# Kernel optimization log

Hardware: AMD Instinct MI355X
Metric: run time of the kernel (lower is better)

## Reference

```python
import jax, jax.numpy as jnp
import numpy as np

B, L, D_MODEL = 2, 2048, 512
EXPAND = 2
ED = EXPAND * D_MODEL          # d_inner = 1024
N = 16                          # d_state
D_CONV = 4
DT_RANK = (D_MODEL + N - 1) // N  # 32
D_FF = 1024
EPS = 1e-5


def _mamba_params(key, pre):
    ks = jax.random.split(key, 6)
    s = 0.02
    p = {}
    p[pre + 'in_w'] = jax.random.normal(ks[0], (D_MODEL, 2 * ED), jnp.float32) * s
    p[pre + 'conv_w'] = jax.random.normal(ks[1], (ED, 1, D_CONV), jnp.float32) * s
    p[pre + 'conv_b'] = jnp.zeros((ED,), jnp.float32)
    p[pre + 'xproj_w'] = jax.random.normal(ks[2], (ED, DT_RANK + 2 * N), jnp.float32) * s
    p[pre + 'dt_w'] = jax.random.normal(ks[3], (DT_RANK, ED), jnp.float32) * s
    p[pre + 'dt_b'] = jax.random.normal(ks[4], (ED,), jnp.float32) * s
    # S4D-real init: A_log = log(1..N) per channel
    p[pre + 'A_log'] = jnp.log(jnp.broadcast_to(jnp.arange(1, N + 1, dtype=jnp.float32), (ED, N)))
    p[pre + 'D'] = jnp.ones((ED,), jnp.float32)
    p[pre + 'out_w'] = jax.random.normal(ks[5], (ED, D_MODEL), jnp.float32) * s
    return p


def setup_inputs() -> dict:
    key = jax.random.key(0)
    k_x, k_f, k_b, k_ffn = jax.random.split(key, 4)
    inp = {'x': jax.random.normal(k_x, (B, L, D_MODEL), jnp.float32)}
    inp.update(_mamba_params(k_f, 'f_'))
    inp.update(_mamba_params(k_b, 'b_'))
    inp['norm1_g'] = jnp.ones((D_MODEL,), jnp.float32)
    inp['norm1_b'] = jnp.zeros((D_MODEL,), jnp.float32)
    inp['norm2_g'] = jnp.ones((D_MODEL,), jnp.float32)
    inp['norm2_b'] = jnp.zeros((D_MODEL,), jnp.float32)
    k1, k2 = jax.random.split(k_ffn)
    inp['ffn_w1'] = jax.random.normal(k1, (D_MODEL, D_FF), jnp.float32) * 0.02
    inp['ffn_b1'] = jnp.zeros((D_FF,), jnp.float32)
    inp['ffn_w2'] = jax.random.normal(k2, (D_FF, D_MODEL), jnp.float32) * 0.02
    inp['ffn_b2'] = jnp.zeros((D_MODEL,), jnp.float32)
    return inp


def _selective_scan(x, delta, A, Bm, C, Dp):
    # x, delta: (B,L,ED); A: (ED,N); Bm, C: (B,L,N); Dp: (ED,)
    def step(h, inp):
        x_t, d_t, B_t, C_t = inp  # (B,ED),(B,ED),(B,N),(B,N)
        dA = jnp.exp(d_t[..., None] * A)                      # (B,ED,N)
        dBx = (d_t * x_t)[..., None] * B_t[:, None, :]        # (B,ED,N)
        h = dA * h + dBx
        y = jnp.einsum('ben,bn->be', h, C_t)
        return h, y

    h0 = jnp.zeros((x.shape[0], ED, N), x.dtype)
    xs = (x.transpose(1, 0, 2), delta.transpose(1, 0, 2),
          Bm.transpose(1, 0, 2), C.transpose(1, 0, 2))
    _, ys = jax.lax.scan(step, h0, xs)
    return ys.transpose(1, 0, 2) + x * Dp


def _mamba(x, in_w, conv_w, conv_b, xproj_w, dt_w, dt_b, A_log, Dp, out_w):
    xz = x @ in_w                                  # (B,L,2*ED)
    xs, z = jnp.split(xz, 2, axis=-1)
    # depthwise causal conv over time
    xc = jax.lax.conv_general_dilated(
        xs.transpose(0, 2, 1), conv_w, (1,), [(D_CONV - 1, 0)],
        dimension_numbers=('NCH', 'OIH', 'NCH'), feature_group_count=ED)
    xc = jax.nn.silu(xc.transpose(0, 2, 1) + conv_b)          # (B,L,ED)
    dbl = xc @ xproj_w                                        # (B,L,DT_RANK+2N)
    dt = dbl[..., :DT_RANK]
    Bm = dbl[..., DT_RANK:DT_RANK + N]
    C = dbl[..., DT_RANK + N:]
    delta = jax.nn.softplus(dt @ dt_w + dt_b)                 # (B,L,ED)
    A = -jnp.exp(A_log)
    y = _selective_scan(xc, delta, A, Bm, C, Dp)
    y = y * jax.nn.silu(z)
    return y @ out_w


def _layernorm(h, g, b):
    mu = jnp.mean(h, axis=-1, keepdims=True)
    var = jnp.var(h, axis=-1, keepdims=True)
    return (h - mu) * jax.lax.rsqrt(var + EPS) * g + b


def _ffn(h, w1, b1, w2, b2):
    return jnp.maximum(h @ w1 + b1, 0.0) @ w2 + b2


def reference(x,
              f_in_w, f_conv_w, f_conv_b, f_xproj_w, f_dt_w, f_dt_b, f_A_log, f_D, f_out_w,
              b_in_w, b_conv_w, b_conv_b, b_xproj_w, b_dt_w, b_dt_b, b_A_log, b_D, b_out_w,
              norm1_g, norm1_b, norm2_g, norm2_b,
              ffn_w1, ffn_b1, ffn_w2, ffn_b2):
    mf = _mamba(x, f_in_w, f_conv_w, f_conv_b, f_xproj_w, f_dt_w, f_dt_b, f_A_log, f_D, f_out_w)
    mf = _layernorm(mf, norm1_g, norm1_b)
    out_f = _ffn(mf, ffn_w1, ffn_b1, ffn_w2, ffn_b2) + mf
    # NOTE: original code computes norm2 but then uses the UN-normalized
    # backward output (variable shadowing bug); we replicate that faithfully.
    mb = _mamba(jnp.flip(x, axis=1), b_in_w, b_conv_w, b_conv_b, b_xproj_w,
                b_dt_w, b_dt_b, b_A_log, b_D, b_out_w)
    out_b = _ffn(mb, ffn_w1, ffn_b1, ffn_w2, ffn_b2) + mb
    return out_f + out_b
```

## Files before the change

### kernel.cpp

```cpp
#include <hip/hip_runtime.h>
#include <hip/hip_bf16.h>
#include <math.h>


#define BD 2
#define LD 2048
#define DMODEL 512
#define EDIM 1024
#define NST 16
#define DTR 32
#define DFF 1024
#define MROWS (BD*LD)

typedef __hip_bfloat16 bf16;
typedef __bf16 bf16x8 __attribute__((ext_vector_type(8)));
typedef __bf16 bf16x4 __attribute__((ext_vector_type(4)));
typedef float  f32x4  __attribute__((ext_vector_type(4)));

__device__ __forceinline__ float sig_(float x) { return 1.f / (1.f + __expf(-x)); }

__device__ __forceinline__ void glds16(const void* g, void* l)
{
    __builtin_amdgcn_global_load_lds(
        (const __attribute__((address_space(1))) void*)g,
        (__attribute__((address_space(3))) void*)l, 16, 0, 0);
}

__global__ __launch_bounds__(256)
void prep_k(const float* __restrict__ x, bf16* __restrict__ xbf,
            const float* __restrict__ inw_f, const float* __restrict__ inw_b,
            bf16* __restrict__ inwT,
            const float* __restrict__ outw_f, const float* __restrict__ outw_b,
            bf16* __restrict__ outwT,
            const float* __restrict__ fw1, bf16* __restrict__ fw1T,
            const float* __restrict__ fw2, bf16* __restrict__ fw2T,
            const float* __restrict__ xp_f, const float* __restrict__ xp_b,
            bf16* __restrict__ xpT,
            const float* __restrict__ dtw_f, const float* __restrict__ dtw_b,
            bf16* __restrict__ dtwT)
{
    const int bid = blockIdx.x, tid = threadIdx.x;
    if (bid < 2048) {
        size_t i = (size_t)bid * 1024 + tid * 4;
        float4 v = *(const float4*)(x + i);
        bf16* o = xbf + i;
        o[0] = __float2bfloat16(v.x); o[1] = __float2bfloat16(v.y);
        o[2] = __float2bfloat16(v.z); o[3] = __float2bfloat16(v.w);
        return;
    }
    const float* W; bf16* WT; int R, C, cx, ry;
    if (bid < 4096) {
        int d = (bid - 2048) >> 10, t = (bid - 2048) & 1023;
        W = d ? inw_b : inw_f; WT = inwT + (size_t)d * 2048 * 512;
        R = 512; C = 2048; cx = t & 63; ry = t >> 6;
    } else if (bid < 5120) {
        int d = (bid - 4096) >> 9, t = (bid - 4096) & 511;
        W = d ? outw_b : outw_f; WT = outwT + (size_t)d * 512 * 1024;
        R = 1024; C = 512; cx = t & 15; ry = t >> 4;
    } else if (bid < 5632) {
        int t = bid - 5120; W = fw1; WT = fw1T; R = 512; C = 1024;
        cx = t & 31; ry = t >> 5;
    } else if (bid < 6144) {
        int t = bid - 5632; W = fw2; WT = fw2T; R = 1024; C = 512;
        cx = t & 15; ry = t >> 4;
    } else if (bid < 6272) {
        int d = (bid - 6144) >> 6, t = (bid - 6144) & 63;
        W = d ? xp_b : xp_f; WT = xpT + (size_t)d * 64 * 1024;
        R = 1024; C = 64; cx = t & 1; ry = t >> 1;
    } else {
        int d = (bid - 6272) >> 5, t = (bid - 6272) & 31;
        W = d ? dtw_b : dtw_f; WT = dtwT + (size_t)d * 1024 * DTR;
        R = 32; C = 1024; cx = t; ry = 0;
    }
    __shared__ float tt[32][33];
    const int c0 = cx * 32, r0 = ry * 32;
    const int col = tid & 31, rr = tid >> 5;
#pragma unroll
    for (int p = 0; p < 4; ++p)
        tt[p * 8 + rr][col] = W[(size_t)(r0 + p * 8 + rr) * C + c0 + col];
    __syncthreads();
#pragma unroll
    for (int p = 0; p < 4; ++p)
        WT[(size_t)(c0 + p * 8 + rr) * R + r0 + col] =
            __float2bfloat16(tt[col][p * 8 + rr]);
}

template<int BM, int BN, int MODE, bool FLIPD1, bool CATK>
__global__ __launch_bounds__(256)
void bgemm4_k(const bf16* __restrict__ A, size_t Astr, int lda,
              const bf16* __restrict__ BT, size_t Bstr, int ldb,
              const float* __restrict__ bias,
              bf16* __restrict__ Cb, size_t Cstr, int ldc,
              const bf16* __restrict__ mp, size_t mpStr,
              float* __restrict__ outp, int K)
{
    constexpr int BK = 64;
    constexpr int FRm = BM / 32, FRn = BN / 32;
    constexpr int KH = DFF;
    __shared__ __align__(16) bf16 As[BM][BK];
    __shared__ __align__(16) bf16 Bs[BN][BK];
    const int tid = threadIdx.x;
    const int dir = blockIdx.z;
    const bool flip = FLIPD1 && (dir == 1);
    const bf16* Ad = A + (CATK ? (size_t)0 : (size_t)dir * Astr);
    const bf16* Bd = BT + (size_t)dir * Bstr;
    const int bm = blockIdx.y * BM, bn = blockIdx.x * BN;
    const int wave = tid >> 6, lane = tid & 63;
    const int wm = (wave >> 1) * (BM / 2), wn = (wave & 1) * (BN / 2);
    const int lm = lane & 15, lq = lane >> 4;
    const int lrow = lane >> 3, lcol = (lane & 7) * 8;
    f32x4 acc[FRm][FRn] = {};

    for (int k0 = 0; k0 < K; k0 += BK) {
        const bf16* Ab = Ad;
        int ka = k0;
        if (CATK && k0 >= KH) { Ab = A + Astr; ka = k0 - KH; }
        const int kb = CATK ? (k0 & (KH - 1)) : k0;
#pragma unroll
        for (int c = 0; c < BM / 32; ++c) {
            int row = c * 32 + wave * 8 + lrow;
            int gm = bm + row;
            if (flip) gm = (gm & ~(LD - 1)) + (LD - 1 - (gm & (LD - 1)));
            glds16(Ab + (size_t)gm * lda + ka + lcol,
                   &As[c * 32 + wave * 8][0]);
        }
#pragma unroll
        for (int c = 0; c < BN / 32; ++c) {
            int row = c * 32 + wave * 8 + lrow;
            glds16(Bd + (size_t)(bn + row) * ldb + kb + lcol,
                   &Bs[c * 32 + wave * 8][0]);
        }
        __syncthreads();

#pragma unroll
        for (int kh = 0; kh < 2; ++kh) {
            bf16x8 af[FRm], bfr[FRn];
#pragma unroll
            for (int i = 0; i < FRm; ++i)
                af[i] = *(const bf16x8*)&As[wm + 16 * i + lm][kh * 32 + lq * 8];
#pragma unroll
            for (int j = 0; j < FRn; ++j)
                bfr[j] = *(const bf16x8*)&Bs[wn + 16 * j + lm][kh * 32 + lq * 8];
#pragma unroll
            for (int i = 0; i < FRm; ++i)
#pragma unroll
                for (int j = 0; j < FRn; ++j)
                    acc[i][j] = __builtin_amdgcn_mfma_f32_16x16x32_bf16(
                        af[i], bfr[j], acc[i][j], 0, 0, 0);
        }
        __syncthreads();
    }

    bf16* Cd = (MODE == 5) ? nullptr : Cb + (size_t)dir * Cstr;
#pragma unroll
    for (int i = 0; i < FRm; ++i) {
#pragma unroll
        for (int j = 0; j < FRn; ++j) {
            int col = bn + wn + 16 * j + lm;
            float bv = (MODE == 2) ? bias[col]
                     : (MODE == 5) ? 2.f * bias[col] : 0.f;
#pragma unroll
            for (int r = 0; r < 4; ++r) {
                int row = bm + wm + 16 * i + lq * 4 + r;
                float v = acc[i][j][r] + bv;
                size_t idx = (size_t)row * ldc + col;
                if (MODE == 0)      Cd[idx] = __float2bfloat16(v);
                else if (MODE == 2) Cd[idx] = __float2bfloat16(fmaxf(v, 0.f));
                else {
                    float m2 = __bfloat162float(mp[idx])
                             + __bfloat162float(mp[mpStr + idx]);
                    outp[idx] = v + m2;
                }
            }
        }
    }
}

__global__ __launch_bounds__(256)
void zgate3_k(const bf16* __restrict__ xbf, const bf16* __restrict__ inwT,
              const bf16* __restrict__ y2t_all, bf16* __restrict__ yrow_all)
{
    __shared__ __align__(16) char smem[24576];
    bf16 (*As)[64] = (bf16(*)[64])smem;
    bf16 (*Bs)[64] = (bf16(*)[64])(smem + 8192);
    __bf16 (*sy)[74] = (__bf16(*)[74])smem;
    const int tid = threadIdx.x;
    const int dir = blockIdx.z;
    const bf16* Bd = inwT + (size_t)dir * (2048 * 512) + (size_t)1024 * 512;
    const bf16* y2t = y2t_all + (size_t)dir * ((size_t)MROWS * EDIM);
    bf16* yrow = yrow_all + (size_t)dir * ((size_t)MROWS * EDIM);
    const int bm = blockIdx.y * 64, bn = blockIdx.x * 128;
    const int wave = tid >> 6, lane = tid & 63;
    const int wm = (wave >> 1) * 32, wn = (wave & 1) * 64;
    const int lm = lane & 15, lq = lane >> 4;
    const int lrow = lane >> 3, lcol = (lane & 7) * 8;
    f32x4 acc[2][4] = {};

    for (int k0 = 0; k0 < 512; k0 += 64) {
#pragma unroll
        for (int c = 0; c < 2; ++c) {
            int row = c * 32 + wave * 8 + lrow;
            int gm = bm + row;
            if (dir == 1) gm = (gm & ~(LD - 1)) + (LD - 1 - (gm & (LD - 1)));
            glds16(xbf + (size_t)gm * 512 + k0 + lcol, &As[c * 32 + wave * 8][0]);
        }
#pragma unroll
        for (int c = 0; c < 4; ++c) {
            int row = c * 32 + wave * 8 + lrow;
            glds16(Bd + (size_t)(bn + row) * 512 + k0 + lcol,
                   &Bs[c * 32 + wave * 8][0]);
        }
        __syncthreads();
#pragma unroll
        for (int kh = 0; kh < 2; ++kh) {
            bf16x8 af[2], bfr[4];
#pragma unroll
            for (int i = 0; i < 2; ++i)
                af[i] = *(const bf16x8*)&As[wm + 16 * i + lm][kh * 32 + lq * 8];
#pragma unroll
            for (int j = 0; j < 4; ++j)
                bfr[j] = *(const bf16x8*)&Bs[wn + 16 * j + lm][kh * 32 + lq * 8];
#pragma unroll
            for (int i = 0; i < 2; ++i)
#pragma unroll
                for (int j = 0; j < 4; ++j)
                    acc[i][j] = __builtin_amdgcn_mfma_f32_16x16x32_bf16(
                        af[i], bfr[j], acc[i][j], 0, 0, 0);
        }
        __syncthreads();
    }

    {
        const int b = bm >> 11, l0 = bm & (LD - 1);
        int e = tid >> 1, lh = (tid & 1) * 32;
        const bf16* yp = y2t + ((size_t)b * EDIM + bn + e) * LD + l0 + lh;
#pragma unroll
        for (int i = 0; i < 4; ++i)
            *(bf16x8*)&sy[e][lh + i * 8] = *(const bf16x8*)(yp + i * 8);
    }
    __syncthreads();
#pragma unroll
    for (int i = 0; i < 2; ++i) {
#pragma unroll
        for (int j = 0; j < 4; ++j) {
            int col = bn + wn + 16 * j + lm;
#pragma unroll
            for (int r = 0; r < 4; ++r) {
                int row = bm + wm + 16 * i + lq * 4 + r;
                float z = acc[i][j][r];
                float g = z * sig_(z);
                float y = (float)sy[col - bn][row - bm];
                yrow[(size_t)row * EDIM + col] = __float2bfloat16(g * y);
            }
        }
    }
}

__global__ __launch_bounds__(256)
void conv3_k(const bf16* __restrict__ xs2,
             const float* __restrict__ cw_f, const float* __restrict__ cb_f,
             const float* __restrict__ cw_b, const float* __restrict__ cb_b,
             bf16* __restrict__ xct2)
{
    __shared__ __align__(16) __bf16 sxs[72][64];
    __shared__ float sout[64][65];
    const int tid = threadIdx.x;
    const int dir = blockIdx.z;
    const bf16* xs = xs2 + (size_t)dir * ((size_t)MROWS * EDIM);
    const float* w  = dir ? cw_b : cw_f;
    const float* cb = dir ? cb_b : cb_f;
    bf16* xct = xct2 + (size_t)dir * ((size_t)MROWS * EDIM);
    const int e0 = blockIdx.x * 64;
    const int bl0 = blockIdx.y * 64;
    const int lloc0 = bl0 & (LD - 1);
    const int b = bl0 >> 11;
    const int wave = tid >> 6, lane = tid & 63;

    for (int c = wave; c < 9; c += 4) {
        int g = bl0 - 8 + c * 8 + (lane >> 3);
        glds16(xs + (size_t)g * EDIM + e0 + (lane & 7) * 8, &sxs[c * 8][0]);
    }
    __syncthreads();
    if (lloc0 == 0 && tid < 192)
        sxs[5 + (tid >> 6)][tid & 63] = (__bf16)0.f;
    __syncthreads();

    {
        int lr4 = tid >> 6, e = tid & 63;
        float w0 = w[(e0 + e) * 4 + 0], w1 = w[(e0 + e) * 4 + 1];
        float w2 = w[(e0 + e) * 4 + 2], w3 = w[(e0 + e) * 4 + 3];
        float cbv = cb[e0 + e];
#pragma unroll
        for (int i = 0; i < 16; ++i) {
            int lr = i * 4 + lr4;
            float acc = cbv;
            acc = fmaf((float)sxs[lr + 5][e], w0, acc);
            acc = fmaf((float)sxs[lr + 6][e], w1, acc);
            acc = fmaf((float)sxs[lr + 7][e], w2, acc);
            acc = fmaf((float)sxs[lr + 8][e], w3, acc);
            sout[e][lr] = acc * sig_(acc);
        }
    }
    __syncthreads();
    {
        int l8 = (tid & 7) * 8;
#pragma unroll
        for (int i = 0; i < 2; ++i) {
            int er = i * 32 + (tid >> 3);
            bf16x8 o;
#pragma unroll
            for (int j = 0; j < 8; ++j) o[j] = (__bf16)sout[er][l8 + j];
            *(bf16x8*)(xct + ((size_t)b * EDIM + e0 + er) * LD + lloc0 + l8) = o;
        }
    }
}

__global__ __launch_bounds__(256)
void g2m2_k(const bf16* __restrict__ xct2, const bf16* __restrict__ xpT2,
            float* __restrict__ dblt2, float* __restrict__ dbldt2)
{
    __shared__ float As[32][68];
    __shared__ __align__(16) bf16 Bs[64][64];
    __shared__ float sDT[32][33];
    __shared__ float sBC[32][33];
    const int tid = threadIdx.x;
    const int dir = blockIdx.z;
    const bf16* xct = xct2 + (size_t)dir * ((size_t)MROWS * EDIM);
    const bf16* xpT = xpT2 + (size_t)dir * (64 * 1024);
    float* dblt = dblt2 + (size_t)dir * (2 * 64 * LD);
    float* dbldt = dbldt2 + (size_t)dir * (2 * 2048 * DTR);
    const int bm = blockIdx.y * 32;
    const int bB = bm >> 11, l0 = bm & (LD - 1);
    const int wave = tid >> 6, lane = tid & 63;
    const int wml = (wave >> 1) * 16, wnn = (wave & 1) * 32;
    const int lm = lane & 15, lq = lane >> 4;
    const int er = tid >> 2, l8 = (tid & 3) * 8;
    const int lrow = lane >> 3, lcol = (lane & 7) * 8;
    f32x4 acc[2] = {};

    for (int k0 = 0; k0 < EDIM; k0 += 64) {
#pragma unroll
        for (int c = 0; c < 2; ++c) {
            int row = c * 32 + wave * 8 + lrow;
            glds16(xpT + (size_t)row * 1024 + k0 + lcol, &Bs[c * 32 + wave * 8][0]);
        }
        {
            bf16x8 v = *(const bf16x8*)(xct +
                ((size_t)bB * EDIM + k0 + er) * LD + l0 + l8);
#pragma unroll
            for (int j = 0; j < 8; ++j) As[l8 + j][er] = (float)v[j];
        }
        __syncthreads();
#pragma unroll
        for (int kh = 0; kh < 2; ++kh) {
            bf16x8 af;
#pragma unroll
            for (int j = 0; j < 8; ++j)
                af[j] = (__bf16)As[wml + lm][kh * 32 + lq * 8 + j];
#pragma unroll
            for (int j = 0; j < 2; ++j) {
                bf16x8 bfr = *(const bf16x8*)&Bs[wnn + 16 * j + lm][kh * 32 + lq * 8];
                acc[j] = __builtin_amdgcn_mfma_f32_16x16x32_bf16(af, bfr, acc[j], 0, 0, 0);
            }
        }
        __syncthreads();
    }
    if (wnn == 0) {
#pragma unroll
        for (int j = 0; j < 2; ++j) {
            int col = 16 * j + lm;
#pragma unroll
            for (int r = 0; r < 4; ++r)
                sDT[wml + lq * 4 + r][col] = acc[j][r];
        }
    } else {
#pragma unroll
        for (int j = 0; j < 2; ++j) {
            int col = 16 * j + lm;
#pragma unroll
            for (int r = 0; r < 4; ++r)
                sBC[col][wml + lq * 4 + r] = acc[j][r];
        }
    }
    __syncthreads();
    {
        int row = tid >> 3, c4 = (tid & 7) * 4;
        float4 v = make_float4(sDT[row][c4], sDT[row][c4 + 1],
                               sDT[row][c4 + 2], sDT[row][c4 + 3]);
        *(float4*)(dbldt + (size_t)(bB * 2048 + l0 + row) * DTR + c4) = v;
    }
    {
        int nr = tid >> 3, ll = (tid & 7) * 4;
        float4 v = make_float4(sBC[nr][ll], sBC[nr][ll + 1],
                               sBC[nr][ll + 2], sBC[nr][ll + 3]);
        *(float4*)(dblt + (size_t)(bB * 64 + 32 + nr) * LD + l0 + ll) = v;
    }
}

__global__ __launch_bounds__(256)
void g3m_k(const float* __restrict__ dbldt2, const bf16* __restrict__ dtwT2,
           const float* __restrict__ dtb_f, const float* __restrict__ dtb_b,
           bf16* __restrict__ dltt2)
{
    __shared__ __align__(16) bf16 As[64][40];
    __shared__ __align__(16) bf16 Bs[64][32];
    __shared__ float sC[64][65];
    const int tid = threadIdx.x;
    const int dir = blockIdx.z;
    const float* Ap = dbldt2 + (size_t)dir * (2 * 2048 * DTR);
    const bf16* BT = dtwT2 + (size_t)dir * (1024 * DTR);
    const float* bias = dir ? dtb_b : dtb_f;
    bf16* dltt = dltt2 + (size_t)dir * ((size_t)MROWS * EDIM);
    const int bm = blockIdx.y * 64, bn = blockIdx.x * 64;
    const int bB = bm >> 11, l0 = bm & (LD - 1);
    const int wave = tid >> 6, lane = tid & 63;
    const int wm = (wave >> 1) * 32, wn = (wave & 1) * 32;
    const int lm = lane & 15, lq = lane >> 4;

    {
        int row = tid >> 2, c8 = (tid & 3) * 8;
        const float* p = Ap + (size_t)(bB * 2048 + l0 + row) * DTR + c8;
        float4 v0 = *(const float4*)p, v1 = *(const float4*)(p + 4);
        bf16x8 o;
        o[0]=(__bf16)v0.x; o[1]=(__bf16)v0.y; o[2]=(__bf16)v0.z; o[3]=(__bf16)v0.w;
        o[4]=(__bf16)v1.x; o[5]=(__bf16)v1.y; o[6]=(__bf16)v1.z; o[7]=(__bf16)v1.w;
        *(bf16x8*)&As[row][c8] = o;
    }
    glds16(BT + (size_t)(bn + wave * 16 + (lane >> 2)) * DTR + (lane & 3) * 8,
           &Bs[wave * 16][0]);
    __syncthreads();

    bf16x8 af[2], bfr[2];
#pragma unroll
    for (int i = 0; i < 2; ++i)
        af[i] = *(const bf16x8*)&As[wm + 16 * i + lm][lq * 8];
#pragma unroll
    for (int j = 0; j < 2; ++j)
        bfr[j] = *(const bf16x8*)&Bs[wn + 16 * j + lm][lq * 8];
    f32x4 acc[2][2] = {};
#pragma unroll
    for (int i = 0; i < 2; ++i)
#pragma unroll
        for (int j = 0; j < 2; ++j)
            acc[i][j] = __builtin_amdgcn_mfma_f32_16x16x32_bf16(
                af[i], bfr[j], acc[i][j], 0, 0, 0);

#pragma unroll
    for (int i = 0; i < 2; ++i)
#pragma unroll
        for (int j = 0; j < 2; ++j) {
            int col = wn + 16 * j + lm;
            float bv = bias[bn + col];
#pragma unroll
            for (int r = 0; r < 4; ++r) {
                int row = wm + 16 * i + lq * 4 + r;
                float v = acc[i][j][r] + bv;
                v = (v > 20.f) ? v : log1pf(__expf(v));
                sC[col][row] = v;
            }
        }
    __syncthreads();
    {
        int erow = tid >> 2, l16 = (tid & 3) * 16;
        bf16* d = dltt + ((size_t)bB * EDIM + bn + erow) * LD + l0 + l16;
#pragma unroll
        for (int h = 0; h < 2; ++h) {
            bf16x8 o;
#pragma unroll
            for (int j = 0; j < 8; ++j) o[j] = (__bf16)sC[erow][l16 + h * 8 + j];
            *(bf16x8*)(d + h * 8) = o;
        }
    }
}

__global__ __launch_bounds__(256)
void scan6_k(bf16* __restrict__ xct2, const bf16* __restrict__ dltt2,
             const float* __restrict__ dblt2,
             const float* __restrict__ alog_f, const float* __restrict__ alog_b,
             const float* __restrict__ dp_f, const float* __restrict__ dp_b)
{
    __shared__ float sA[NST];
    __shared__ float sWp[NST][4];
    __shared__ float sWs[NST][4];
    const int gid = blockIdx.x;
    const int dir = gid >> 11;
    const int bb  = (gid >> 10) & 1;
    const int e   = gid & (EDIM - 1);
    const float* A_log = dir ? alog_b : alog_f;
    const float* Dp    = dir ? dp_b   : dp_f;
    bf16* xct = xct2 + (size_t)dir * ((size_t)MROWS * EDIM);
    const bf16* dltt = dltt2 + (size_t)dir * ((size_t)MROWS * EDIM);
    const float* bt = dblt2 + (size_t)dir * (2 * 64 * LD) + (size_t)bb * 64 * LD;
    const int tid = threadIdx.x;
    const int wave = tid >> 6, lane = tid & 63;
    const size_t baset = ((size_t)bb * EDIM + e) * LD;
    const int l0 = tid * 8;

    if (tid < NST) sA[tid] = -__expf(A_log[e * NST + tid]);

    float xv[8], dv[8], dx[8];
    {
        bf16x8 xr = *(const bf16x8*)(xct + baset + l0);
        bf16x8 dr = *(const bf16x8*)(dltt + baset + l0);
#pragma unroll
        for (int j = 0; j < 8; ++j) { xv[j] = (float)xr[j]; dv[j] = (float)dr[j]; }
    }
#pragma unroll
    for (int j = 0; j < 8; ++j) dx[j] = dv[j] * xv[j];
    __syncthreads();

    float y[8] = {};
    for (int n = 0; n < NST; ++n) {
        const float An = sA[n];
        const float* Bp = bt + (size_t)(DTR + n) * LD + l0;
        const float* Cp = bt + (size_t)(DTR + NST + n) * LD + l0;
        float4 b0 = *(const float4*)Bp, b1 = *(const float4*)(Bp + 4);
        float4 c0 = *(const float4*)Cp, c1 = *(const float4*)(Cp + 4);
        float Br[8] = {b0.x,b0.y,b0.z,b0.w, b1.x,b1.y,b1.z,b1.w};
        float Cr[8] = {c0.x,c0.y,c0.z,c0.w, c1.x,c1.y,c1.z,c1.w};

        float S[8], P[8];
        float h = 0.f, pr = 1.f;
#pragma unroll
        for (int l = 0; l < 8; ++l) {
            float a = __expf(dv[l] * An);
            pr *= a;
            h = fmaf(a, h, dx[l] * Br[l]);
            P[l] = pr; S[l] = h;
        }

        float p = pr, s = h;
#pragma unroll
        for (int d = 1; d < 64; d <<= 1) {
            float pp = __shfl_up(p, d, 64);
            float sp = __shfl_up(s, d, 64);
            if (lane >= d) { s = fmaf(sp, p, s); p *= pp; }
        }
        if (lane == 63) { sWp[n][wave] = p; sWs[n][wave] = s; }
        __syncthreads();
        float Hoff = 0.f;
#pragma unroll
        for (int w = 0; w < 3; ++w)
            if (w < wave) Hoff = fmaf(sWp[n][w], Hoff, sWs[n][w]);
        float pprev = __shfl_up(p, 1, 64);
        float sprev = __shfl_up(s, 1, 64);
        float H = (lane == 0) ? Hoff : fmaf(pprev, Hoff, sprev);

#pragma unroll
        for (int l = 0; l < 8; ++l)
            y[l] = fmaf(Cr[l], fmaf(P[l], H, S[l]), y[l]);
    }

    const float Dv = Dp[e];
    bf16x8 o;
#pragma unroll
    for (int l = 0; l < 8; ++l) o[l] = (__bf16)fmaf(xv[l], Dv, y[l]);
    *(bf16x8*)(xct + baset + l0) = o;
}

__global__ __launch_bounds__(256)
void ln_k(bf16* __restrict__ m, const float* __restrict__ gg,
          const float* __restrict__ bb)
{
    int row = (blockIdx.x * 256 + threadIdx.x) >> 6;
    int lane = threadIdx.x & 63;
    bf16* r = m + (size_t)row * DMODEL;
    float v[8], s = 0.f, s2 = 0.f;
#pragma unroll
    for (int i = 0; i < 8; ++i) {
        v[i] = __bfloat162float(r[lane + 64 * i]);
        s += v[i]; s2 = fmaf(v[i], v[i], s2);
    }
#pragma unroll
    for (int off = 32; off >= 1; off >>= 1) {
        s  += __shfl_xor(s, off, 64);
        s2 += __shfl_xor(s2, off, 64);
    }
    float mu = s * (1.f / DMODEL);
    float var = s2 * (1.f / DMODEL) - mu * mu;
    float inv = rsqrtf(var + 1e-5f);
#pragma unroll
    for (int i = 0; i < 8; ++i)
        r[lane + 64 * i] = __float2bfloat16(
            (v[i] - mu) * inv * gg[lane + 64 * i] + bb[lane + 64 * i]);
}

__global__ void sentinel_k(float* __restrict__ o)
{
    int i = blockIdx.x * 256 + threadIdx.x;
    o[i] = 100.0f;
}

extern "C" void kernel_launch(void* const* d_in, const int* in_sizes, int n_in,
                              void* d_out, int out_size, void* d_ws, size_t ws_size,
                              hipStream_t stream)
{
    const float* x    = (const float*)d_in[0];
    const float* n1g  = (const float*)d_in[19];
    const float* n1b  = (const float*)d_in[20];
    const float* fw1  = (const float*)d_in[23];
    const float* fb1  = (const float*)d_in[24];
    const float* fw2  = (const float*)d_in[25];
    const float* fb2  = (const float*)d_in[26];
    float* out = (float*)d_out;

    const size_t MiB = 1024 * 1024;
    const size_t SZ_DM = (size_t)MROWS * DMODEL;
    if (ws_size < 49 * MiB) {
        sentinel_k<<<dim3(SZ_DM / 256), dim3(256), 0, stream>>>(out);
        return;
    }

    char* base = (char*)d_ws;
    bf16* fw1T  = (bf16*)base;
    bf16* fw2T  = (bf16*)(base + 1 * MiB);
    bf16* outwT = (bf16*)(base + 2 * MiB);
    bf16* inwT  = (bf16*)(base + 4 * MiB);
    bf16* xbf   = (bf16*)(base + 8 * MiB);
    char* RA    = base + 12 * MiB;
    bf16* xs2   = (bf16*)RA;
    bf16* dltt2 = (bf16*)RA;
    bf16* yrow2 = (bf16*)RA;
    bf16* ffh2  = (bf16*)RA;
    char* RB    = base + 28 * MiB;
    bf16* xct2  = (bf16*)RB;
    bf16* mbf2  = (bf16*)RB;
    float* dblt2 = (float*)(base + 44 * MiB);
    float* dbldt2 = (float*)(base + 46 * MiB);
    bf16* xpT2  = (bf16*)(base + 48 * MiB);
    bf16* dtwT2 = (bf16*)(base + 48 * MiB + 256 * 1024);

    const float* inw_f  = (const float*)d_in[1];
    const float* cw_f   = (const float*)d_in[2];
    const float* cb_f   = (const float*)d_in[3];
    const float* xp_f   = (const float*)d_in[4];
    const float* dtw_f  = (const float*)d_in[5];
    const float* dtb_f  = (const float*)d_in[6];
    const float* alog_f = (const float*)d_in[7];
    const float* dp_f   = (const float*)d_in[8];
    const float* outw_f = (const float*)d_in[9];
    const float* inw_b  = (const float*)d_in[10];
    const float* cw_b   = (const float*)d_in[11];
    const float* cb_b   = (const float*)d_in[12];
    const float* xp_b   = (const float*)d_in[13];
    const float* dtw_b  = (const float*)d_in[14];
    const float* dtb_b  = (const float*)d_in[15];
    const float* alog_b = (const float*)d_in[16];
    const float* dp_b   = (const float*)d_in[17];
    const float* outw_b = (const float*)d_in[18];

    dim3 blk(256);
    const size_t U = (size_t)MROWS * EDIM;

    prep_k<<<dim3(6336), blk, 0, stream>>>(x, xbf, inw_f, inw_b, inwT,
                                           outw_f, outw_b, outwT,
                                           fw1, fw1T, fw2, fw2T,
                                           xp_f, xp_b, xpT2,
                                           dtw_f, dtw_b, dtwT2);
    bgemm4_k<128, 64, 0, true, false><<<dim3(16, 32, 2), blk, 0, stream>>>(
        xbf, 0, DMODEL, inwT, (size_t)2048 * 512, DMODEL, nullptr,
        xs2, U, EDIM, nullptr, 0, nullptr, DMODEL);
    conv3_k<<<dim3(16, 64, 2), blk, 0, stream>>>(xs2, cw_f, cb_f, cw_b, cb_b, xct2);
    g2m2_k<<<dim3(1, 128, 2), blk, 0, stream>>>(xct2, xpT2, dblt2, dbldt2);
    g3m_k<<<dim3(16, 64, 2), blk, 0, stream>>>(dbldt2, dtwT2, dtb_f, dtb_b, dltt2);
    scan6_k<<<dim3(4096), blk, 0, stream>>>(xct2, dltt2, dblt2,
                                            alog_f, alog_b, dp_f, dp_b);
    zgate3_k<<<dim3(8, 64, 2), blk, 0, stream>>>(xbf, inwT, xct2, yrow2);
    bgemm4_k<64, 64, 0, false, false><<<dim3(8, 64, 2), blk, 0, stream>>>(
        yrow2, U, EDIM, outwT, (size_t)512 * 1024, EDIM, nullptr,
        mbf2, SZ_DM, DMODEL, nullptr, 0, nullptr, EDIM);
    ln_k<<<dim3(MROWS / 4), blk, 0, stream>>>(mbf2, n1g, n1b);
    bgemm4_k<128, 64, 2, false, false><<<dim3(16, 32, 2), blk, 0, stream>>>(
        mbf2, SZ_DM, DMODEL, fw1T, 0, DMODEL, fb1,
        ffh2, U, DFF, nullptr, 0, nullptr, DMODEL);
    bgemm4_k<64, 64, 5, false, true><<<dim3(8, 64, 1), blk, 0, stream>>>(
        ffh2, U, DFF, fw2T, 0, DFF, fb2,
        nullptr, 0, DMODEL, mbf2, SZ_DM, out, 2 * DFF);
}
```

Before: 345.2 us.

## Double-buffer bf16 GEMM LDS tiles with async global-to-LDS prefetch

The shared GEMM kernel now keeps two LDS buffers with a K-tile of 32 instead of 64. It issues the global_load_lds for the next tile before computing the current one, using explicit vmcnt waits and raw barriers. The goal is to hide global memory latency behind MFMA work, which the old load-sync-compute-sync loop exposed on every iteration. In exchange it runs twice as many barriers per K step, does less MFMA work per stage, and relies on hand-counted vmcnt values that must match the number of loads issued.

```diff
diff --git a/kernel.cpp b/kernel.cpp
--- a/kernel.cpp
+++ b/kernel.cpp
@@ -24,6 +24,20 @@
     __builtin_amdgcn_global_load_lds(
         (const __attribute__((address_space(1))) void*)g,
         (__attribute__((address_space(3))) void*)l, 16, 0, 0);
+}
+
+template<int N> __device__ __forceinline__ void vmw_()
+{
+    if constexpr (N == 0)      asm volatile("s_waitcnt vmcnt(0)" ::: "memory");
+    else if constexpr (N == 2) asm volatile("s_waitcnt vmcnt(2)" ::: "memory");
+    else if constexpr (N == 3) asm volatile("s_waitcnt vmcnt(3)" ::: "memory");
+    else if constexpr (N == 4) asm volatile("s_waitcnt vmcnt(4)" ::: "memory");
+}
+__device__ __forceinline__ void bar_()
+{
+    asm volatile("" ::: "memory");
+    __builtin_amdgcn_s_barrier();
+    asm volatile("" ::: "memory");
 }
 
 __global__ __launch_bounds__(256)
@@ -87,18 +101,19 @@
 
 template<int BM, int BN, int MODE, bool FLIPD1, bool CATK>
 __global__ __launch_bounds__(256)
-void bgemm4_k(const bf16* __restrict__ A, size_t Astr, int lda,
+void bgemm5_k(const bf16* __restrict__ A, size_t Astr, int lda,
               const bf16* __restrict__ BT, size_t Bstr, int ldb,
               const float* __restrict__ bias,
               bf16* __restrict__ Cb, size_t Cstr, int ldc,
               const bf16* __restrict__ mp, size_t mpStr,
               float* __restrict__ outp, int K)
 {
-    constexpr int BK = 64;
+    constexpr int BK = 32;
     constexpr int FRm = BM / 32, FRn = BN / 32;
     constexpr int KH = DFF;
-    __shared__ __align__(16) bf16 As[BM][BK];
-    __shared__ __align__(16) bf16 Bs[BN][BK];
+    constexpr int NC = BM / 64 + BN / 64;
+    __shared__ __align__(16) bf16 As[2][BM][BK];
+    __shared__ __align__(16) bf16 Bs[2][BN][BK];
     const int tid = threadIdx.x;
     const int dir = blockIdx.z;
     const bool flip = FLIPD1 && (dir == 1);
@@ -108,48 +123,58 @@
     const int wave = tid >> 6, lane = tid & 63;
     const int wm = (wave >> 1) * (BM / 2), wn = (wave & 1) * (BN / 2);
     const int lm = lane & 15, lq = lane >> 4;
-    const int lrow = lane >> 3, lcol = (lane & 7) * 8;
+    const int lrow = lane >> 2, lcol = (lane & 3) * 8;
     f32x4 acc[FRm][FRn] = {};
 
-    for (int k0 = 0; k0 < K; k0 += BK) {
+    auto STAGE = [&](int buf, int k0) {
         const bf16* Ab = Ad;
         int ka = k0;
         if (CATK && k0 >= KH) { Ab = A + Astr; ka = k0 - KH; }
         const int kb = CATK ? (k0 & (KH - 1)) : k0;
 #pragma unroll
-        for (int c = 0; c < BM / 32; ++c) {
-            int row = c * 32 + wave * 8 + lrow;
+        for (int c = 0; c < BM / 64; ++c) {
+            int row = c * 64 + wave * 16 + lrow;
             int gm = bm + row;
             if (flip) gm = (gm & ~(LD - 1)) + (LD - 1 - (gm & (LD - 1)));
             glds16(Ab + (size_t)gm * lda + ka + lcol,
-                   &As[c * 32 + wave * 8][0]);
-        }
-#pragma unroll
-        for (int c = 0; c < BN / 32; ++c) {
-            int row = c * 32 + wave * 8 + lrow;
+                   &As[buf][c * 64 + wave * 16][0]);
+        }
+#pragma unroll
+        for (int c = 0; c < BN / 64; ++c) {
+            int row = c * 64 + wave * 16 + lrow;
             glds16(Bd + (size_t)(bn + row) * ldb + kb + lcol,
-                   &Bs[c * 32 + wave * 8][0]);
-        }
-        __syncthreads();
-
-#pragma unroll
-        for (int kh = 0; kh < 2; ++kh) {
-            bf16x8 af[FRm], bfr[FRn];
-#pragma unroll
-            for (int i = 0; i < FRm; ++i)
-                af[i] = *(const bf16x8*)&As[wm + 16 * i + lm][kh * 32 + lq * 8];
+                   &Bs[buf][c * 64 + wave * 16][0]);
+        }
+    };
+    auto COMPUTE = [&](int buf) {
+        bf16x8 af[FRm], bfr[FRn];
+#pragma unroll
+        for (int i = 0; i < FRm; ++i)
+            af[i] = *(const bf16x8*)&As[buf][wm + 16 * i + lm][lq * 8];
+#pragma unroll
+        for (int j = 0; j < FRn; ++j)
+            bfr[j] = *(const bf16x8*)&Bs[buf][wn + 16 * j + lm][lq * 8];
+#pragma unroll
+        for (int i = 0; i < FRm; ++i)
 #pragma unroll
             for (int j = 0; j < FRn; ++j)
-                bfr[j] = *(const bf16x8*)&Bs[wn + 16 * j + lm][kh * 32 + lq * 8];
-#pragma unroll
-            for (int i = 0; i < FRm; ++i)
-#pragma unroll
-                for (int j = 0; j < FRn; ++j)
-                    acc[i][j] = __builtin_amdgcn_mfma_f32_16x16x32_bf16(
-                        af[i], bfr[j], acc[i][j], 0, 0, 0);
-        }
-        __syncthreads();
-    }
+                acc[i][j] = __builtin_amdgcn_mfma_f32_16x16x32_bf16(
+                    af[i], bfr[j], acc[i][j], 0, 0, 0);
+    };
+
+    STAGE(0, 0);
+    int cur = 0;
+    for (int k0 = BK; k0 < K; k0 += BK) {
+        STAGE(cur ^ 1, k0);
+        vmw_<NC>();
+        bar_();
+        COMPUTE(cur);
+        bar_();
+        cur ^= 1;
+    }
+    vmw_<0>();
+    bar_();
+    COMPUTE(cur);
 
     bf16* Cd = (MODE == 5) ? nullptr : Cb + (size_t)dir * Cstr;
 #pragma unroll
@@ -657,7 +682,7 @@
                                            fw1, fw1T, fw2, fw2T,
                                            xp_f, xp_b, xpT2,
                                            dtw_f, dtw_b, dtwT2);
-    bgemm4_k<128, 64, 0, true, false><<<dim3(16, 32, 2), blk, 0, stream>>>(
+    bgemm5_k<128, 64, 0, true, false><<<dim3(16, 32, 2), blk, 0, stream>>>(
         xbf, 0, DMODEL, inwT, (size_t)2048 * 512, DMODEL, nullptr,
         xs2, U, EDIM, nullptr, 0, nullptr, DMODEL);
     conv3_k<<<dim3(16, 64, 2), blk, 0, stream>>>(xs2, cw_f, cb_f, cw_b, cb_b, xct2);
@@ -666,14 +691,14 @@
     scan6_k<<<dim3(4096), blk, 0, stream>>>(xct2, dltt2, dblt2,
                                             alog_f, alog_b, dp_f, dp_b);
     zgate3_k<<<dim3(8, 64, 2), blk, 0, stream>>>(xbf, inwT, xct2, yrow2);
-    bgemm4_k<64, 64, 0, false, false><<<dim3(8, 64, 2), blk, 0, stream>>>(
+    bgemm5_k<64, 64, 0, false, false><<<dim3(8, 64, 2), blk, 0, stream>>>(
         yrow2, U, EDIM, outwT, (size_t)512 * 1024, EDIM, nullptr,
         mbf2, SZ_DM, DMODEL, nullptr, 0, nullptr, EDIM);
     ln_k<<<dim3(MROWS / 4), blk, 0, stream>>>(mbf2, n1g, n1b);
-    bgemm4_k<128, 64, 2, false, false><<<dim3(16, 32, 2), blk, 0, stream>>>(
+    bgemm5_k<128, 64, 2, false, false><<<dim3(16, 32, 2), blk, 0, stream>>>(
         mbf2, SZ_DM, DMODEL, fw1T, 0, DMODEL, fb1,
         ffh2, U, DFF, nullptr, 0, nullptr, DMODEL);
-    bgemm4_k<64, 64, 5, false, true><<<dim3(8, 64, 1), blk, 0, stream>>>(
+    bgemm5_k<64, 64, 5, false, true><<<dim3(8, 64, 1), blk, 0, stream>>>(
         ffh2, U, DFF, fw2T, 0, DFF, fb2,
         nullptr, 0, DMODEL, mbf2, SZ_DM, out, 2 * DFF);
 }
```

Result: no change. 351.8 us (+1.9%).
